# Kernel optimization log

Measured on AMD Instinct MI355X. Metric: run time of the kernel, lower is better.

Reference implementation:

```python
import jax, jax.numpy as jnp
import numpy as np

N_NODES = 100000
N_EDGES = 1600000
IN_FEATS = 32
OUT_FEATS = 32


def setup_inputs() -> dict:
    key = jax.random.key(0)
    ks = jax.random.split(key, 7)
    x = jax.random.normal(ks[0], (N_NODES, IN_FEATS), dtype=jnp.float32)
    src = jax.random.randint(ks[1], (N_EDGES,), 0, N_NODES, dtype=jnp.int32)
    dst = jax.random.randint(ks[2], (N_EDGES,), 0, N_NODES, dtype=jnp.int32)
    # torch nn.LSTMCell params: weight_ih [4H, in], weight_hh [4H, H], biases [4H]
    s_ih = 1.0 / np.sqrt(OUT_FEATS)
    W_ih = jax.random.uniform(ks[3], (4 * OUT_FEATS, IN_FEATS), jnp.float32, -s_ih, s_ih)
    W_hh = jax.random.uniform(ks[4], (4 * OUT_FEATS, OUT_FEATS), jnp.float32, -s_ih, s_ih)
    b_ih = jax.random.uniform(ks[5], (4 * OUT_FEATS,), jnp.float32, -s_ih, s_ih)
    b_hh = jax.random.uniform(ks[6], (4 * OUT_FEATS,), jnp.float32, -s_ih, s_ih)
    return {"x": x, "src": src, "dst": dst, "W_ih": W_ih, "W_hh": W_hh,
            "b_ih": b_ih, "b_hh": b_hh}


def _tgcn_cell(x, src, dst, W_ih, W_hh, b_ih, b_hh):
    n = x.shape[0]
    # dropout is identity in eval mode (self.training=False)
    # copy_src + sum: gather per-edge messages x[src], sum into dst nodes
    h_agg = jax.ops.segment_sum(x[src], dst, num_segments=n)  # [N, in]
    # LSTMCell with zero initial (h0, c0); gate order in torch: i, f, g, o
    gates = h_agg @ W_ih.T + b_ih + b_hh  # h0 = 0 -> h0 @ W_hh.T == 0
    H = W_hh.shape[1]
    i, f, g, o = (gates[:, :H], gates[:, H:2 * H],
                  gates[:, 2 * H:3 * H], gates[:, 3 * H:])
    c = jax.nn.sigmoid(i) * jnp.tanh(g)  # f * c0 = 0
    h = jax.nn.sigmoid(o) * jnp.tanh(c)
    return jax.nn.relu(h)  # activf


def reference(x, src, dst, W_ih, W_hh, b_ih, b_hh):
    return _tgcn_cell(x, src, dst, W_ih, W_hh, b_ih, b_hh)
```

## Files before the change

### kernel.cpp

```cpp
#include <hip/hip_runtime.h>


constexpr int NN   = 100000;
constexpr int NE   = 1600000;
constexpr int F    = 32;
constexpr int NSB  = 50;
constexpr int NPSB = 2000;
constexpr int CAP1 = 34816;
constexpr int EPA  = 3200;
constexpr int NBA  = NE / EPA;
constexpr int NPB  = 50;
constexpr int NBIN = NN / NPB;
constexpr int BPSB = NPSB / NPB;
constexpr int CHUNK = 2048;
constexpr int NCH  = CAP1 / CHUNK;
constexpr int CAP2 = 1024;
static_assert(NSB * NPSB == NN, "superbin geometry");
static_assert(NBIN * NPB == NN, "bin geometry");
static_assert(NBA * EPA == NE, "edge partition");
static_assert(NCH * CHUNK == CAP1, "chunking");

__global__ __launch_bounds__(256) void pA(
    const int* __restrict__ src, const int* __restrict__ dst,
    unsigned int* __restrict__ seg1, int* __restrict__ fill1)
{
    __shared__ int hist[NSB], sbase[NSB], gbase[NSB];
    __shared__ unsigned int stg[EPA];
    __shared__ unsigned char bid[EPA];

    const int t  = threadIdx.x;
    const int e0 = blockIdx.x * EPA;

    for (int i = t; i < NSB; i += 256) hist[i] = 0;
    __syncthreads();

    int rS[13], rD[13], rR[13];
    #pragma unroll
    for (int j = 0; j < 13; ++j) {
        int e = e0 + t + j * 256;
        if (e < e0 + EPA) {
            int d = dst[e];
            rS[j] = src[e];
            rD[j] = d;
            rR[j] = atomicAdd(&hist[(unsigned)d / NPSB], 1);
        }
    }
    __syncthreads();

    if (t == 0) { int acc = 0; for (int b = 0; b < NSB; ++b) { sbase[b] = acc; acc += hist[b]; } }
    __syncthreads();

    if (t < NSB) { int c = hist[t]; gbase[t] = c ? atomicAdd(&fill1[t], c) : 0; }
    __syncthreads();

    #pragma unroll
    for (int j = 0; j < 13; ++j) {
        int e = e0 + t + j * 256;
        if (e < e0 + EPA) {
            unsigned d = (unsigned)rD[j];
            unsigned sb = d / NPSB, dl2 = d - sb * NPSB;
            int lp  = sbase[sb] + rR[j];
            stg[lp] = ((unsigned)rS[j] << 11) | dl2;
            bid[lp] = (unsigned char)sb;
        }
    }
    __syncthreads();

    for (int p = t; p < EPA; p += 256) {
        int b    = bid[p];
        int slot = gbase[b] + (p - sbase[b]);
        if (slot < CAP1) seg1[(size_t)b * CAP1 + slot] = stg[p];
    }
}

__global__ __launch_bounds__(256) void pB(
    const unsigned int* __restrict__ seg1, const int* __restrict__ fill1,
    unsigned int* __restrict__ seg2, int* __restrict__ fill2)
{
    __shared__ int hist[BPSB], sbase[BPSB], gbase[BPSB];
    __shared__ unsigned int stg[CHUNK];
    __shared__ unsigned char bid[CHUNK];

    const int t  = threadIdx.x;
    const int sb = blockIdx.x / NCH;
    const int ch = blockIdx.x % NCH;

    int n1 = fill1[sb]; if (n1 > CAP1) n1 = CAP1;
    int cnt = n1 - ch * CHUNK;
    if (cnt <= 0) return;
    if (cnt > CHUNK) cnt = CHUNK;
    const unsigned int* sg = seg1 + (size_t)sb * CAP1 + ch * CHUNK;

    if (t < BPSB) hist[t] = 0;
    __syncthreads();

    unsigned rV[8]; int rR[8];
    #pragma unroll
    for (int j = 0; j < 8; ++j) {
        int i = t + j * 256;
        if (i < cnt) {
            unsigned v = sg[i];
            rV[j] = v;
            rR[j] = atomicAdd(&hist[(v & 2047u) / NPB], 1);
        }
    }
    __syncthreads();

    if (t == 0) { int acc = 0; for (int b = 0; b < BPSB; ++b) { sbase[b] = acc; acc += hist[b]; } }
    __syncthreads();

    if (t < BPSB) { int c = hist[t]; gbase[t] = c ? atomicAdd(&fill2[sb * BPSB + t], c) : 0; }
    __syncthreads();

    #pragma unroll
    for (int j = 0; j < 8; ++j) {
        int i = t + j * 256;
        if (i < cnt) {
            unsigned v = rV[j];
            unsigned s = v >> 11, dl2 = v & 2047u;
            unsigned lb = dl2 / NPB, dl = dl2 - lb * NPB;
            int lp  = sbase[lb] + rR[j];
            stg[lp] = (s << 8) | dl;
            bid[lp] = (unsigned char)lb;
        }
    }
    __syncthreads();

    for (int p = t; p < cnt; p += 256) {
        int b    = bid[p];
        int slot = gbase[b] + (p - sbase[b]);
        if (slot < CAP2) seg2[(size_t)(sb * BPSB + b) * CAP2 + slot] = stg[p];
    }
}

__device__ __forceinline__ float sigm(float v)  { return 1.0f / (1.0f + __expf(-v)); }
__device__ __forceinline__ float tanh_(float v) { return 1.0f - 2.0f / (__expf(2.0f * v) + 1.0f); }

__global__ __launch_bounds__(256) void p2(
    const float* __restrict__ x,
    const unsigned int* __restrict__ seg2, const int* __restrict__ fill2,
    const float* __restrict__ W,
    const float* __restrict__ b_ih, const float* __restrict__ b_hh,
    float* __restrict__ out)
{
    __shared__ float hs[NPB * F];
    __shared__ float Ws[96 * 33];
    __shared__ float bs[96];
    __shared__ unsigned int sgl[CAP2];
    __shared__ int cnt[NPB], start[NPB];

    const int t   = threadIdx.x;
    const int bin = blockIdx.x;

    for (int i = t; i < 96 * 32; i += 256) {
        int r = i >> 5, k = i & 31;
        int sr = (r < 32) ? r : r + 32;
        Ws[r * 33 + k] = W[sr * 32 + k];
    }
    if (t < 96) { int sr = (t < 32) ? t : t + 32; bs[t] = b_ih[sr] + b_hh[sr]; }
    if (t < NPB) cnt[t] = 0;
    __syncthreads();

    int nE = fill2[bin]; if (nE > CAP2) nE = CAP2;
    const unsigned int* s2 = seg2 + (size_t)bin * CAP2;

    unsigned rV[4]; int rR[4];
    #pragma unroll
    for (int j = 0; j < 4; ++j) {
        int i = t + j * 256;
        if (i < nE) { unsigned v = s2[i]; rV[j] = v; rR[j] = atomicAdd(&cnt[v & 255u], 1); }
    }
    __syncthreads();

    if (t == 0) { int acc = 0; for (int b = 0; b < NPB; ++b) { start[b] = acc; acc += cnt[b]; } }
    __syncthreads();

    #pragma unroll
    for (int j = 0; j < 4; ++j) {
        int i = t + j * 256;
        if (i < nE) { unsigned v = rV[j]; sgl[start[v & 255u] + rR[j]] = v; }
    }
    __syncthreads();

    const int lane = t & 31, g = t >> 5;
    for (int dl = g; dl < NPB; dl += 8) {
        int st = start[dl], cn = cnt[dl];
        float acc = 0.0f;
        for (int b = 0; b < cn; b += 16) {
            float xv[16];
            #pragma unroll
            for (int k = 0; k < 16; ++k) {
                int idx = b + k; if (idx > cn - 1) idx = cn - 1;
                unsigned v = sgl[st + idx];
                xv[k] = x[(v >> 8) * F + lane];
            }
            #pragma unroll
            for (int k = 0; k < 16; ++k) acc += (b + k < cn) ? xv[k] : 0.0f;
        }
        hs[dl * F + lane] = acc;
    }
    __syncthreads();

    for (int i = t; i < NPB * F; i += 256) {
        int node = i >> 5, j = i & 31;
        const float* h  = &hs[node * F];
        const float* wi = &Ws[j * 33];
        const float* wg = &Ws[(32 + j) * 33];
        const float* wo = &Ws[(64 + j) * 33];
        float ai = bs[j], ag = bs[32 + j], ao = bs[64 + j];
        #pragma unroll
        for (int k = 0; k < F; ++k) {
            float hv = h[k];
            ai += hv * wi[k];
            ag += hv * wg[k];
            ao += hv * wo[k];
        }
        float c  = sigm(ai) * tanh_(ag);
        float hh = sigm(ao) * tanh_(c);
        out[(bin * NPB + node) * F + j] = fmaxf(hh, 0.0f);
    }
}

extern "C" void kernel_launch(void* const* d_in, const int* in_sizes, int n_in,
                              void* d_out, int out_size, void* d_ws, size_t ws_size,
                              hipStream_t stream) {
    const float* x    = (const float*)d_in[0];
    const int*   src  = (const int*)  d_in[1];
    const int*   dst  = (const int*)  d_in[2];
    const float* W_ih = (const float*)d_in[3];
    const float* b_ih = (const float*)d_in[5];
    const float* b_hh = (const float*)d_in[6];
    float* out = (float*)d_out;

    unsigned int* seg1 = (unsigned int*)d_ws;
    unsigned int* seg2 = seg1 + (size_t)NSB * CAP1;
    int* fill1 = (int*)(seg2 + (size_t)NBIN * CAP2);
    int* fill2 = fill1 + 64;

    hipMemsetAsync(fill1, 0, (64 + NBIN) * sizeof(int), stream);
    pA<<<NBA,       256, 0, stream>>>(src, dst, seg1, fill1);
    pB<<<NSB * NCH, 256, 0, stream>>>(seg1, fill1, seg2, fill2);
    p2<<<NBIN,      256, 0, stream>>>(x, seg2, fill2, W_ih, b_ih, b_hh, out);
}
```

Measured before the change: 158.7 us.

## Drop second partition pass; bins filter superbin lists directly with XCD swizzle

Removes the pB kernel and the seg2 buffer. Each final p2 block now scans its whole superbin list twice, once to build a per-node histogram of matching entries and once to scatter them into shared memory. Block indices are swizzled so that bins of the same superbin land on the same XCD and can reuse its L2. The first pass also moves to int4 loads, a smaller edge tile per block and a wavefront shuffle prefix scan. This saves one launch and one global write/read round trip, but each superbin segment is now read redundantly by all 40 of its bins.

Measured after the change: 256.0 us. +61.3%, slower.

```diff
diff --git a/kernel.cpp b/kernel.cpp
--- a/kernel.cpp
+++ b/kernel.cpp
@@ -7,18 +7,17 @@
 constexpr int NSB  = 50;
 constexpr int NPSB = 2000;
 constexpr int CAP1 = 34816;
-constexpr int EPA  = 3200;
+constexpr int EPA  = 1600;
 constexpr int NBA  = NE / EPA;
 constexpr int NPB  = 50;
 constexpr int NBIN = NN / NPB;
 constexpr int BPSB = NPSB / NPB;
-constexpr int CHUNK = 2048;
-constexpr int NCH  = CAP1 / CHUNK;
 constexpr int CAP2 = 1024;
 static_assert(NSB * NPSB == NN, "superbin geometry");
 static_assert(NBIN * NPB == NN, "bin geometry");
 static_assert(NBA * EPA == NE, "edge partition");
-static_assert(NCH * CHUNK == CAP1, "chunking");
+static_assert(EPA % 4 == 0 && (EPA / 4) <= 512, "int4 load geometry");
+static_assert(NBIN % 8 == 0, "bijective XCD swizzle");
 
 __global__ __launch_bounds__(256) void pA(
     const int* __restrict__ src, const int* __restrict__ dst,
@@ -31,37 +30,60 @@
     const int t  = threadIdx.x;
     const int e0 = blockIdx.x * EPA;
 
-    for (int i = t; i < NSB; i += 256) hist[i] = 0;
-    __syncthreads();
-
-    int rS[13], rD[13], rR[13];
+    if (t < NSB) hist[t] = 0;
+    __syncthreads();
+
+    const int4* s4p = reinterpret_cast<const int4*>(src + e0);
+    const int4* d4p = reinterpret_cast<const int4*>(dst + e0);
+    int4 s4[2], d4[2];
+    int  rR[8];
+
     #pragma unroll
-    for (int j = 0; j < 13; ++j) {
-        int e = e0 + t + j * 256;
-        if (e < e0 + EPA) {
-            int d = dst[e];
-            rS[j] = src[e];
-            rD[j] = d;
-            rR[j] = atomicAdd(&hist[(unsigned)d / NPSB], 1);
-        }
-    }
-    __syncthreads();
-
-    if (t == 0) { int acc = 0; for (int b = 0; b < NSB; ++b) { sbase[b] = acc; acc += hist[b]; } }
+    for (int j = 0; j < 2; ++j) {
+        int idx = t + j * 256;
+        if (idx < EPA / 4) { s4[j] = s4p[idx]; d4[j] = d4p[idx]; }
+    }
+    #pragma unroll
+    for (int j = 0; j < 2; ++j) {
+        int idx = t + j * 256;
+        if (idx < EPA / 4) {
+            const int* dd = &d4[j].x;
+            #pragma unroll
+            for (int k = 0; k < 4; ++k)
+                rR[j * 4 + k] = atomicAdd(&hist[(unsigned)dd[k] / NPSB], 1);
+        }
+    }
+    __syncthreads();
+
+    if (t < 64) {
+        int v = (t < NSB) ? hist[t] : 0;
+        int incl = v;
+        #pragma unroll
+        for (int off = 1; off < 64; off <<= 1) {
+            int u = __shfl_up(incl, off, 64);
+            if (t >= off) incl += u;
+        }
+        if (t < NSB) sbase[t] = incl - v;
+    }
     __syncthreads();
 
     if (t < NSB) { int c = hist[t]; gbase[t] = c ? atomicAdd(&fill1[t], c) : 0; }
     __syncthreads();
 
     #pragma unroll
-    for (int j = 0; j < 13; ++j) {
-        int e = e0 + t + j * 256;
-        if (e < e0 + EPA) {
-            unsigned d = (unsigned)rD[j];
-            unsigned sb = d / NPSB, dl2 = d - sb * NPSB;
-            int lp  = sbase[sb] + rR[j];
-            stg[lp] = ((unsigned)rS[j] << 11) | dl2;
-            bid[lp] = (unsigned char)sb;
+    for (int j = 0; j < 2; ++j) {
+        int idx = t + j * 256;
+        if (idx < EPA / 4) {
+            const int* dd = &d4[j].x;
+            const int* ss = &s4[j].x;
+            #pragma unroll
+            for (int k = 0; k < 4; ++k) {
+                unsigned d  = (unsigned)dd[k];
+                unsigned sb = d / NPSB, dl2 = d - sb * NPSB;
+                int lp  = sbase[sb] + rR[j * 4 + k];
+                stg[lp] = ((unsigned)ss[k] << 11) | dl2;
+                bid[lp] = (unsigned char)sb;
+            }
         }
     }
     __syncthreads();
@@ -73,72 +95,12 @@
     }
 }
 
-__global__ __launch_bounds__(256) void pB(
-    const unsigned int* __restrict__ seg1, const int* __restrict__ fill1,
-    unsigned int* __restrict__ seg2, int* __restrict__ fill2)
-{
-    __shared__ int hist[BPSB], sbase[BPSB], gbase[BPSB];
-    __shared__ unsigned int stg[CHUNK];
-    __shared__ unsigned char bid[CHUNK];
-
-    const int t  = threadIdx.x;
-    const int sb = blockIdx.x / NCH;
-    const int ch = blockIdx.x % NCH;
-
-    int n1 = fill1[sb]; if (n1 > CAP1) n1 = CAP1;
-    int cnt = n1 - ch * CHUNK;
-    if (cnt <= 0) return;
-    if (cnt > CHUNK) cnt = CHUNK;
-    const unsigned int* sg = seg1 + (size_t)sb * CAP1 + ch * CHUNK;
-
-    if (t < BPSB) hist[t] = 0;
-    __syncthreads();
-
-    unsigned rV[8]; int rR[8];
-    #pragma unroll
-    for (int j = 0; j < 8; ++j) {
-        int i = t + j * 256;
-        if (i < cnt) {
-            unsigned v = sg[i];
-            rV[j] = v;
-            rR[j] = atomicAdd(&hist[(v & 2047u) / NPB], 1);
-        }
-    }
-    __syncthreads();
-
-    if (t == 0) { int acc = 0; for (int b = 0; b < BPSB; ++b) { sbase[b] = acc; acc += hist[b]; } }
-    __syncthreads();
-
-    if (t < BPSB) { int c = hist[t]; gbase[t] = c ? atomicAdd(&fill2[sb * BPSB + t], c) : 0; }
-    __syncthreads();
-
-    #pragma unroll
-    for (int j = 0; j < 8; ++j) {
-        int i = t + j * 256;
-        if (i < cnt) {
-            unsigned v = rV[j];
-            unsigned s = v >> 11, dl2 = v & 2047u;
-            unsigned lb = dl2 / NPB, dl = dl2 - lb * NPB;
-            int lp  = sbase[lb] + rR[j];
-            stg[lp] = (s << 8) | dl;
-            bid[lp] = (unsigned char)lb;
-        }
-    }
-    __syncthreads();
-
-    for (int p = t; p < cnt; p += 256) {
-        int b    = bid[p];
-        int slot = gbase[b] + (p - sbase[b]);
-        if (slot < CAP2) seg2[(size_t)(sb * BPSB + b) * CAP2 + slot] = stg[p];
-    }
-}
-
 __device__ __forceinline__ float sigm(float v)  { return 1.0f / (1.0f + __expf(-v)); }
 __device__ __forceinline__ float tanh_(float v) { return 1.0f - 2.0f / (__expf(2.0f * v) + 1.0f); }
 
 __global__ __launch_bounds__(256) void p2(
     const float* __restrict__ x,
-    const unsigned int* __restrict__ seg2, const int* __restrict__ fill2,
+    const unsigned int* __restrict__ seg1, const int* __restrict__ fill1,
     const float* __restrict__ W,
     const float* __restrict__ b_ih, const float* __restrict__ b_hh,
     float* __restrict__ out)
@@ -147,10 +109,13 @@
     __shared__ float Ws[96 * 33];
     __shared__ float bs[96];
     __shared__ unsigned int sgl[CAP2];
-    __shared__ int cnt[NPB], start[NPB];
-
-    const int t   = threadIdx.x;
-    const int bin = blockIdx.x;
+    __shared__ int hist[NPB], start_[NPB], cur[NPB];
+
+    const int t    = threadIdx.x;
+    const int bid0 = blockIdx.x;
+    const int bin  = (bid0 & 7) * (NBIN / 8) + (bid0 >> 3);
+    const int sb   = bin / BPSB;
+    const int lo   = (bin % BPSB) * NPB;
 
     for (int i = t; i < 96 * 32; i += 256) {
         int r = i >> 5, k = i & 31;
@@ -158,41 +123,71 @@
         Ws[r * 33 + k] = W[sr * 32 + k];
     }
     if (t < 96) { int sr = (t < 32) ? t : t + 32; bs[t] = b_ih[sr] + b_hh[sr]; }
-    if (t < NPB) cnt[t] = 0;
-    __syncthreads();
-
-    int nE = fill2[bin]; if (nE > CAP2) nE = CAP2;
-    const unsigned int* s2 = seg2 + (size_t)bin * CAP2;
-
-    unsigned rV[4]; int rR[4];
-    #pragma unroll
-    for (int j = 0; j < 4; ++j) {
-        int i = t + j * 256;
-        if (i < nE) { unsigned v = s2[i]; rV[j] = v; rR[j] = atomicAdd(&cnt[v & 255u], 1); }
-    }
-    __syncthreads();
-
-    if (t == 0) { int acc = 0; for (int b = 0; b < NPB; ++b) { start[b] = acc; acc += cnt[b]; } }
-    __syncthreads();
-
-    #pragma unroll
-    for (int j = 0; j < 4; ++j) {
-        int i = t + j * 256;
-        if (i < nE) { unsigned v = rV[j]; sgl[start[v & 255u] + rR[j]] = v; }
+    if (t < NPB) hist[t] = 0;
+    __syncthreads();
+
+    int n1 = fill1[sb]; if (n1 > CAP1) n1 = CAP1;
+    const unsigned int* s1 = seg1 + (size_t)sb * CAP1;
+
+    for (int i0 = 0; i0 < n1; i0 += 1024) {
+        unsigned v[4];
+        #pragma unroll
+        for (int k = 0; k < 4; ++k) {
+            int i = i0 + k * 256 + t;
+            v[k] = (i < n1) ? s1[i] : 0xFFFFFFFFu;
+        }
+        #pragma unroll
+        for (int k = 0; k < 4; ++k) {
+            int dl2 = (int)(v[k] & 2047u);
+            if (dl2 >= lo && dl2 < lo + NPB) atomicAdd(&hist[dl2 - lo], 1);
+        }
+    }
+    __syncthreads();
+
+    if (t < 64) {
+        int vv = (t < NPB) ? hist[t] : 0;
+        int incl = vv;
+        #pragma unroll
+        for (int off = 1; off < 64; off <<= 1) {
+            int u = __shfl_up(incl, off, 64);
+            if (t >= off) incl += u;
+        }
+        if (t < NPB) start_[t] = incl - vv;
+    }
+    __syncthreads();
+    if (t < NPB) cur[t] = start_[t];
+    __syncthreads();
+
+    for (int i0 = 0; i0 < n1; i0 += 1024) {
+        unsigned v[4];
+        #pragma unroll
+        for (int k = 0; k < 4; ++k) {
+            int i = i0 + k * 256 + t;
+            v[k] = (i < n1) ? s1[i] : 0xFFFFFFFFu;
+        }
+        #pragma unroll
+        for (int k = 0; k < 4; ++k) {
+            int dl2 = (int)(v[k] & 2047u);
+            if (dl2 >= lo && dl2 < lo + NPB) {
+                int r = atomicAdd(&cur[dl2 - lo], 1);
+                if (r < CAP2) sgl[r] = v[k] >> 11;
+            }
+        }
     }
     __syncthreads();
 
     const int lane = t & 31, g = t >> 5;
     for (int dl = g; dl < NPB; dl += 8) {
-        int st = start[dl], cn = cnt[dl];
+        int st = start_[dl], cn = hist[dl];
+        if (st >= CAP2) cn = 0; else if (st + cn > CAP2) cn = CAP2 - st;
         float acc = 0.0f;
         for (int b = 0; b < cn; b += 16) {
             float xv[16];
             #pragma unroll
             for (int k = 0; k < 16; ++k) {
                 int idx = b + k; if (idx > cn - 1) idx = cn - 1;
-                unsigned v = sgl[st + idx];
-                xv[k] = x[(v >> 8) * F + lane];
+                unsigned s = sgl[st + idx];
+                xv[k] = x[s * F + lane];
             }
             #pragma unroll
             for (int k = 0; k < 16; ++k) acc += (b + k < cn) ? xv[k] : 0.0f;
@@ -233,12 +228,9 @@
     float* out = (float*)d_out;
 
     unsigned int* seg1 = (unsigned int*)d_ws;
-    unsigned int* seg2 = seg1 + (size_t)NSB * CAP1;
-    int* fill1 = (int*)(seg2 + (size_t)NBIN * CAP2);
-    int* fill2 = fill1 + 64;
-
-    hipMemsetAsync(fill1, 0, (64 + NBIN) * sizeof(int), stream);
-    pA<<<NBA,       256, 0, stream>>>(src, dst, seg1, fill1);
-    pB<<<NSB * NCH, 256, 0, stream>>>(seg1, fill1, seg2, fill2);
-    p2<<<NBIN,      256, 0, stream>>>(x, seg2, fill2, W_ih, b_ih, b_hh, out);
+    int* fill1 = (int*)(seg1 + (size_t)NSB * CAP1);
+
+    hipMemsetAsync(fill1, 0, NSB * sizeof(int), stream);
+    pA<<<NBA,  256, 0, stream>>>(src, dst, seg1, fill1);
+    p2<<<NBIN, 256, 0, stream>>>(x, seg1, fill1, W_ih, b_ih, b_hh, out);
 }
```
